# Optimization experiments

Measured on AMD Instinct MI355X. Metric: run time of the kernel, lower is better.

## Reference

```python
import jax, jax.numpy as jnp
import numpy as np

N_HEAD = 16
EPS = 1e-5


def setup_inputs() -> dict:
    key = jax.random.key(0)
    ks = jax.random.split(key, 9)
    B, T, C = 2, 1024, 1024
    s = 0.02
    return {
        "x": jax.random.normal(ks[0], (B, T, C), jnp.float32),
        "Wq": jax.random.normal(ks[1], (C, C), jnp.float32) * s,
        "Wk": jax.random.normal(ks[2], (C, C), jnp.float32) * s,
        "Wv": jax.random.normal(ks[3], (C, C), jnp.float32) * s,
        "Wq2": jax.random.normal(ks[4], (C, C), jnp.float32) * s,
        "Wk2": jax.random.normal(ks[5], (C, C), jnp.float32) * s,
        "Wo": jax.random.normal(ks[6], (C, C), jnp.float32) * s,
        "mixture": jnp.full((1,), -5.0, jnp.float32),  # quartet_gate_init
        "quartet_scale": jnp.ones((1,), jnp.float32),
    }


def reference(x, Wq, Wk, Wv, Wq2, Wk2, Wo, mixture, quartet_scale):
    B, T, C = x.shape
    H = N_HEAD
    Dh = C // H
    scale = 1.0 / jnp.sqrt(jnp.asarray(Dh, x.dtype))

    def heads(W):
        # torch Linear: y = x @ W.T ; then view(B,T,H,Dh).transpose(1,2)
        return (x @ W.T).reshape(B, T, H, Dh).transpose(0, 2, 1, 3)  # [B,H,T,Dh]

    q, k, v = heads(Wq), heads(Wk), heads(Wv)
    q2, k2 = heads(Wq2), heads(Wk2)

    qk = jnp.einsum("bhqd,bhkd->bhqk", q, k) * scale      # [B,H,T,T]
    q2k2 = jnp.einsum("bhqd,bhkd->bhqk", q2, k2) * scale  # [B,H,T,T]

    def row_norm(s):
        mu = s.mean(axis=-1, keepdims=True)
        sigma = s.std(axis=-1, keepdims=True, ddof=1)  # torch std is unbiased
        return (s - mu) / (sigma + EPS)

    qk_n = row_norm(qk)
    q2k2_n = row_norm(q2k2)
    m = jax.nn.sigmoid(mixture)  # [1], broadcasts
    scores = (1.0 - m) * qk_n + m * (qk_n * q2k2_n) * quartet_scale

    causal = jnp.tril(jnp.ones((T, T), bool))  # [T,T]
    scores = jnp.where(causal, scores, -jnp.inf)
    attn = jax.nn.softmax(scores, axis=-1)  # [B,H,T,T]

    y = jnp.einsum("bhqk,bhkd->bhqd", attn, v)  # [B,H,T,Dh]
    y = y.transpose(0, 2, 1, 3).reshape(B, T, C)
    return y @ Wo.T
```

## Files before the change

kernel.cpp:

```cpp
#include <hip/hip_runtime.h>
#include <hip/hip_bf16.h>
#include <stdint.h>

#define TS 1024
#define CS 1024
#define NH 16
#define DHEAD 64
#define NBATCH 2
#define EPSV 1e-5f
#define MEG 1048576

typedef __bf16 bf16x8 __attribute__((ext_vector_type(8)));
typedef float  f32x4  __attribute__((ext_vector_type(4)));

#define MFMA(a, b, c) __builtin_amdgcn_mfma_f32_16x16x32_bf16((a), (b), (c), 0, 0, 0)

__device__ __forceinline__ float bf2f(ushort u){
  union { uint32_t i; float f; } v; v.i = ((uint32_t)u) << 16; return v.f;
}
__device__ __forceinline__ ushort f2bf(float f){
  union { float f; uint32_t i; } v; v.f = f;
  uint32_t r = v.i + 0x7FFFu + ((v.i >> 16) & 1u);
  return (ushort)(r >> 16);
}

__device__ __forceinline__ void gl_lds16(const ushort* g, ushort* l) {
  __builtin_amdgcn_global_load_lds(
      (const __attribute__((address_space(1))) void*)g,
      (__attribute__((address_space(3))) void*)l, 16, 0, 0);
}

__global__ __launch_bounds__(256)
void cast_all(const float* __restrict__ x,
              const float* __restrict__ Wq, const float* __restrict__ Wk,
              const float* __restrict__ Wv, const float* __restrict__ Wq2,
              const float* __restrict__ Wk2, const float* __restrict__ Wo,
              ushort* __restrict__ xb, ushort* __restrict__ wcat)
{
  const int XC = 524288, TOT = 2097152;
  for (int idx = blockIdx.x * 256 + threadIdx.x; idx < TOT; idx += 524288) {
    const float* s; ushort* d; int c;
    if (idx < XC) { s = x; d = xb; c = idx; }
    else {
      int r = idx - XC; int w = r >> 18; c = r & 262143;
      switch (w) {
        case 0:  s = Wq;  d = wcat;           break;
        case 1:  s = Wk;  d = wcat + 1*MEG;   break;
        case 2:  s = Wv;  d = wcat + 4*MEG;   break;
        case 3:  s = Wq2; d = wcat + 2*MEG;   break;
        case 4:  s = Wk2; d = wcat + 3*MEG;   break;
        default: s = Wo;  d = wcat + 5*MEG;   break;
      }
    }
    float4 v = *(const float4*)(s + (size_t)c * 4);
    ushort4 o; o.x = f2bf(v.x); o.y = f2bf(v.y); o.z = f2bf(v.z); o.w = f2bf(v.w);
    *(ushort4*)(d + (size_t)c * 4) = o;
  }
}

#define BM 128
#define BN 128
#define BKK 32

__global__ __launch_bounds__(256, 2)
void gemm_proj(const ushort* __restrict__ A, const ushort* __restrict__ Bt,
               ushort* __restrict__ qb, ushort* __restrict__ kb,
               ushort* __restrict__ q2b, ushort* __restrict__ k2b,
               ushort* __restrict__ vtb,
               ushort* __restrict__ ktb, ushort* __restrict__ k2tb)
{
  __shared__ ushort a_s[BM * BKK];
  __shared__ ushort b_s[BN * BKK];

  const int n0 = blockIdx.x * BN;
  const int m0 = blockIdx.y * BM;

  const int t  = threadIdx.x;
  const int w  = t >> 6, l = t & 63;
  const int wr = w >> 1, wc = w & 1;
  const int l15 = l & 15, l4 = l >> 4;

  const int rs = l >> 2;
  const int c8 = (l & 3) * 8;

  f32x4 acc[4][4] = {};

  for (int k0 = 0; k0 < CS; k0 += BKK) {
    #pragma unroll
    for (int j = 0; j < 2; ++j) {
      int ch = w * 2 + j;
      int r  = ch * 16 + rs;
      gl_lds16(&A [(size_t)(m0 + r) * CS + k0 + c8], &a_s[ch * 512]);
      gl_lds16(&Bt[(size_t)(n0 + r) * CS + k0 + c8], &b_s[ch * 512]);
    }
    __syncthreads();

    bf16x8 af[4], bfr[4];
    #pragma unroll
    for (int mi = 0; mi < 4; ++mi)
      af[mi] = *(const bf16x8*)&a_s[(wr * 64 + mi * 16 + l15) * BKK + l4 * 8];
    #pragma unroll
    for (int ni = 0; ni < 4; ++ni)
      bfr[ni] = *(const bf16x8*)&b_s[(wc * 64 + ni * 16 + l15) * BKK + l4 * 8];

    #pragma unroll
    for (int mi = 0; mi < 4; ++mi)
      #pragma unroll
      for (int ni = 0; ni < 4; ++ni)
        acc[mi][ni] = MFMA(af[mi], bfr[ni], acc[mi][ni]);

    __syncthreads();
  }

  #pragma unroll
  for (int mi = 0; mi < 4; ++mi) {
    #pragma unroll
    for (int ni = 0; ni < 4; ++ni) {
      int col  = n0 + wc * 64 + ni * 16 + l15;
      int row0 = m0 + wr * 64 + mi * 16 + l4 * 4;
      int seg  = col >> 10, cc = col & (CS - 1);
      if (seg < 4) {
        ushort* dst = (seg == 0) ? qb : (seg == 1) ? kb : (seg == 2) ? q2b : k2b;
        float sc = (seg & 1) ? 1.f : 0.125f;
        #pragma unroll
        for (int e = 0; e < 4; ++e)
          dst[(size_t)(row0 + e) * CS + cc] = f2bf(acc[mi][ni][e] * sc);
        if (seg == 1 || seg == 3) {
          int bb = row0 >> 10, tt = row0 & (TS - 1);
          int hh = cc >> 6, dd = cc & (DHEAD - 1);
          ushort* td = (seg == 1) ? ktb : k2tb;
          ushort4 o;
          o.x = f2bf(acc[mi][ni][0]); o.y = f2bf(acc[mi][ni][1]);
          o.z = f2bf(acc[mi][ni][2]); o.w = f2bf(acc[mi][ni][3]);
          *(ushort4*)&td[(((size_t)(bb * NH + hh) * DHEAD + dd) * TS) + tt] = o;
        }
      } else {
        int bb = row0 >> 10, tt = row0 & (TS - 1);
        int hh = cc >> 6, dd = cc & (DHEAD - 1);
        ushort4 o;
        o.x = f2bf(acc[mi][ni][0]); o.y = f2bf(acc[mi][ni][1]);
        o.z = f2bf(acc[mi][ni][2]); o.w = f2bf(acc[mi][ni][3]);
        *(ushort4*)&vtb[(((size_t)(bb * NH + hh) * DHEAD + dd) * TS) + tt] = o;
      }
    }
  }
}

__global__ __launch_bounds__(256, 2)
void gemm_out(const ushort* __restrict__ A, const ushort* __restrict__ Bt,
              float* __restrict__ C)
{
  __shared__ ushort a_s[64 * BKK];
  __shared__ ushort b_s[128 * BKK];

  const int n0 = blockIdx.x * 128;
  const int m0 = blockIdx.y * 64;

  const int t  = threadIdx.x;
  const int w  = t >> 6, l = t & 63;
  const int l15 = l & 15, l4 = l >> 4;
  const int rs = l >> 2;
  const int c8 = (l & 3) * 8;

  f32x4 acc[8] = {};

  for (int k0 = 0; k0 < CS; k0 += BKK) {
    gl_lds16(&A[(size_t)(m0 + w * 16 + rs) * CS + k0 + c8], &a_s[w * 512]);
    #pragma unroll
    for (int j = 0; j < 2; ++j) {
      int ch = w * 2 + j;
      gl_lds16(&Bt[(size_t)(n0 + ch * 16 + rs) * CS + k0 + c8], &b_s[ch * 512]);
    }
    __syncthreads();

    bf16x8 af = *(const bf16x8*)&a_s[(w * 16 + l15) * BKK + l4 * 8];
    #pragma unroll
    for (int ni = 0; ni < 8; ++ni) {
      bf16x8 bfr = *(const bf16x8*)&b_s[(ni * 16 + l15) * BKK + l4 * 8];
      acc[ni] = MFMA(af, bfr, acc[ni]);
    }
    __syncthreads();
  }

  #pragma unroll
  for (int ni = 0; ni < 8; ++ni)
    #pragma unroll
    for (int e = 0; e < 4; ++e)
      C[(size_t)(m0 + w * 16 + l4 * 4 + e) * CS + n0 + ni * 16 + l15] = acc[ni][e];
}

__global__ __launch_bounds__(256, 2)
void gram(const ushort* __restrict__ ktb, const ushort* __restrict__ k2tb,
          ushort* __restrict__ g1b, ushort* __restrict__ g2b,
          float* __restrict__ csb)
{
  __shared__ ushort t_s[64 * 128];

  const int mat = blockIdx.x & 1, z = blockIdx.x >> 1;
  const ushort* S = (mat ? k2tb : ktb) + (size_t)z * DHEAD * TS;

  const int t = threadIdx.x, w = t >> 6, l = t & 63;
  const int l15 = l & 15, l4 = l >> 4;

  f32x4 acc[4] = {};
  float csacc = 0.f;

  for (int tt = 0; tt < 8; ++tt) {
    const int t0 = tt * 128;
    __syncthreads();
    #pragma unroll
    for (int i = 0; i < 4; ++i) {
      int issue = w * 4 + i;
      int row = issue * 4 + l4;
      int gs  = l15 ^ (row & 15);
      gl_lds16(&S[(size_t)row * TS + t0 + gs * 8], &t_s[issue * 512]);
    }
    __syncthreads();

    {
      int r = w * 16 + l15;
      #pragma unroll
      for (int j = 0; j < 4; ++j) {
        int gg = ((l4 * 4 + j) ^ (r & 15)) * 8;
        uint4 vv = *(const uint4*)&t_s[r * 128 + gg];
        const ushort* pu = (const ushort*)&vv;
        #pragma unroll
        for (int e2 = 0; e2 < 8; ++e2) csacc += bf2f(pu[e2]);
      }
    }

    #pragma unroll
    for (int ks = 0; ks < 4; ++ks) {
      int ar = w * 16 + l15;
      bf16x8 af = *(const bf16x8*)&t_s[ar * 128 + ((ks * 4 + l4) ^ (ar & 15)) * 8];
      #pragma unroll
      for (int ni = 0; ni < 4; ++ni) {
        int br = ni * 16 + l15;
        bf16x8 bf_ = *(const bf16x8*)&t_s[br * 128 + ((ks * 4 + l4) ^ (br & 15)) * 8];
        acc[ni] = MFMA(af, bf_, acc[ni]);
      }
    }
  }

  csacc += __shfl_xor(csacc, 16);
  csacc += __shfl_xor(csacc, 32);
  if (l4 == 0)
    csb[(mat * 32 + z) * 64 + w * 16 + l15] = csacc;

  ushort* G = (mat ? g2b : g1b) + (size_t)z * 4096;
  #pragma unroll
  for (int ni = 0; ni < 4; ++ni)
    #pragma unroll
    for (int e = 0; e < 4; ++e)
      G[(w * 16 + l4 * 4 + e) * 64 + ni * 16 + l15] = f2bf(acc[ni][e]);
}

__global__ __launch_bounds__(256, 3)
void attn_fused(const ushort* __restrict__ qb, const ushort* __restrict__ kb,
                const ushort* __restrict__ q2b, const ushort* __restrict__ k2b,
                const ushort* __restrict__ vtb, ushort* __restrict__ yb,
                const ushort* __restrict__ g1b, const ushort* __restrict__ g2b,
                const float* __restrict__ csb,
                const float* __restrict__ mixture, const float* __restrict__ qsc)
{
  __shared__ ushort kbuf [2][4096];
  __shared__ ushort k2buf[2][4096];
  __shared__ ushort vbuf [4096];
  __shared__ ushort p_s  [2 * 32 * 40];

  const int idx  = blockIdx.x;
  const int pp   = idx >> 8;
  const int base = idx & 255;
  const int xcd  = base & 7;
  const int mm   = base >> 3;
  const int qq   = mm & 7;
  const int z    = (mm >> 3) * 8 + xcd;
  const int q32  = 31 - (pp * 8 + qq);
  const int b    = z >> 4, h = z & 15;
  const int m0   = q32 * 32;
  const int nkv  = (q32 >> 1) + 1;

  const ushort* Q  = qb  + (size_t)b * TS * CS + h * DHEAD;
  const ushort* Q2 = q2b + (size_t)b * TS * CS + h * DHEAD;
  const ushort* K  = kb  + (size_t)b * TS * CS + h * DHEAD;
  const ushort* K2 = k2b + (size_t)b * TS * CS + h * DHEAD;
  const ushort* Vt = vtb + (size_t)z * DHEAD * TS;
  const ushort* G1 = g1b + (size_t)z * 4096;
  const ushort* G2 = g2b + (size_t)z * 4096;
  ushort* Y = yb + (size_t)b * TS * CS + h * DHEAD;

  const int t = threadIdx.x, w = t >> 6, l = t & 63;
  const int l15 = l & 15, l4 = l >> 4;
  const int r8 = l >> 3, g7 = l & 7;
  const int p  = w >> 1, wr = w & 1;
  const int qrow = wr * 16 + l15;

  const float L2E = 1.44269504f;
  const float gm = 1.f / (1.f + __expf(-mixture[0]));
  const float mq2 = gm * qsc[0] * L2E;
  const float om2 = (1.f - gm) * L2E;

  auto stage_k = [&](int ti, int bs) {
    const int t0 = ti * 64;
    #pragma unroll
    for (int i = 0; i < 2; ++i) {
      int issue = w * 2 + i;
      int row = issue * 8 + r8;
      int gs  = g7 ^ (row & 7);
      gl_lds16(&K [(size_t)(t0 + row) * CS + gs * 8], &kbuf [bs][issue * 512]);
      gl_lds16(&K2[(size_t)(t0 + row) * CS + gs * 8], &k2buf[bs][issue * 512]);
    }
  };
  auto stage_v = [&](int ti) {
    const int t0 = ti * 64;
    #pragma unroll
    for (int i = 0; i < 2; ++i) {
      int issue = w * 2 + i;
      int row = issue * 8 + r8;
      int gs  = g7 ^ (row & 7);
      gl_lds16(&Vt[(size_t)row * TS + t0 + gs * 8], &vbuf[issue * 512]);
    }
  };

  {
    int row = w * 8 + r8;
    int gs  = g7 ^ (row & 7);
    gl_lds16(&Q [(size_t)(m0 + row) * CS + gs * 8], &vbuf[w * 512]);
    gl_lds16(&Q2[(size_t)(m0 + row) * CS + gs * 8], &vbuf[2048 + w * 512]);
  }
  stage_k(0, 0);
  __syncthreads();

  bf16x8 fq[2], fq2[2];
  #pragma unroll
  for (int ks = 0; ks < 2; ++ks) {
    int gg = ((ks * 4 + l4) ^ (qrow & 7)) * 8;
    fq [ks] = *(const bf16x8*)&vbuf[qrow * 64 + gg];
    fq2[ks] = *(const bf16x8*)&vbuf[2048 + qrow * 64 + gg];
  }

  f32x4 U1[4] = {}, U2[4] = {};
  #pragma unroll
  for (int ks = 0; ks < 2; ++ks)
    #pragma unroll
    for (int ni = 0; ni < 4; ++ni) {
      bf16x8 bg = *(const bf16x8*)&G1[(ni * 16 + l15) * 64 + ks * 32 + l4 * 8];
      U1[ni] = MFMA(bg, fq[ks], U1[ni]);
    }
  #pragma unroll
  for (int ks = 0; ks < 2; ++ks)
    #pragma unroll
    for (int ni = 0; ni < 4; ++ni) {
      bf16x8 bg = *(const bf16x8*)&G2[(ni * 16 + l15) * 64 + ks * 32 + l4 * 8];
      U2[ni] = MFMA(bg, fq2[ks], U2[ni]);
    }

  float ssq1 = 0.f, md1 = 0.f, ssq2 = 0.f, md2 = 0.f;
  #pragma unroll
  for (int ni = 0; ni < 4; ++ni) {
    int gsq = (ni * 2 + (l4 >> 1)) ^ (qrow & 7);
    int off = qrow * 64 + gsq * 8 + (l4 & 1) * 4;
    ushort qa[4], qb2[4];
    *(uint2*)qa  = *(const uint2*)&vbuf[off];
    *(uint2*)qb2 = *(const uint2*)&vbuf[2048 + off];
    float c1[4], c2[4];
    *(float4*)c1 = *(const float4*)&csb[z * 64 + ni * 16 + l4 * 4];
    *(float4*)c2 = *(const float4*)&csb[2048 + z * 64 + ni * 16 + l4 * 4];
    #pragma unroll
    for (int e = 0; e < 4; ++e) {
      float qv1 = bf2f(qa[e]), qv2 = bf2f(qb2[e]);
      ssq1 = fmaf(U1[ni][e], qv1, ssq1); md1 = fmaf(qv1, c1[e], md1);
      ssq2 = fmaf(U2[ni][e], qv2, ssq2); md2 = fmaf(qv2, c2[e], md2);
    }
  }
  ssq1 += __shfl_xor(ssq1, 16); md1 += __shfl_xor(md1, 16);
  ssq2 += __shfl_xor(ssq2, 16); md2 += __shfl_xor(md2, 16);
  ssq1 += __shfl_xor(ssq1, 32); md1 += __shfl_xor(md1, 32);
  ssq2 += __shfl_xor(ssq2, 32); md2 += __shfl_xor(md2, 32);

  const float mu1 = md1 * (1.f / TS), mu2 = md2 * (1.f / TS);
  const float va1 = (ssq1 - (float)TS * mu1 * mu1) * (1.f / (TS - 1));
  const float va2 = (ssq2 - (float)TS * mu2 * mu2) * (1.f / (TS - 1));
  const float iv1 = 1.f / (sqrtf(fmaxf(va1, 0.f)) + EPSV);
  const float iv2 = 1.f / (sqrtf(fmaxf(va2, 0.f)) + EPSV);
  __syncthreads();

  float lrow = 0.f;
  f32x4 accO[4] = {};

  for (int i = 0; i < nkv; ++i) {
    const int t0 = i * 64;
    stage_v(i);
    if (i + 1 < nkv) stage_k(i + 1, (i + 1) & 1);

    const ushort* ks_ = kbuf [i & 1];
    const ushort* k2s_= k2buf[i & 1];

    f32x4 a1[2] = {}, a2[2] = {};
    #pragma unroll
    for (int ks = 0; ks < 2; ++ks) {
      bf16x8 bk[2], bk2[2];
      #pragma unroll
      for (int ni = 0; ni < 2; ++ni) {
        int j  = p * 32 + ni * 16 + l15;
        int gg = ((ks * 4 + l4) ^ (j & 7)) * 8;
        bk [ni] = *(const bf16x8*)&ks_ [j * 64 + gg];
        bk2[ni] = *(const bf16x8*)&k2s_[j * 64 + gg];
      }
      #pragma unroll
      for (int ni = 0; ni < 2; ++ni) {
        a1[ni] = MFMA(bk [ni], fq [ks], a1[ni]);
        a2[ni] = MFMA(bk2[ni], fq2[ks], a2[ni]);
      }
    }

    const int grow = m0 + qrow;
    #pragma unroll
    for (int ni = 0; ni < 2; ++ni) {
      float pe[4];
      #pragma unroll
      for (int e = 0; e < 4; ++e) {
        float n1 = (a1[ni][e] - mu1) * iv1;
        float n2 = (a2[ni][e] - mu2) * iv2;
        float sc = n1 * fmaf(mq2, n2, om2);
        float pv = exp2f(sc);
        int gcol = t0 + p * 32 + ni * 16 + l4 * 4 + e;
        pv = (gcol <= grow) ? pv : 0.f;
        lrow += pv;
        pe[e] = pv;
      }
      uint32_t pk01, pk23;
      asm("v_cvt_pk_bf16_f32 %0, %1, %2" : "=v"(pk01) : "v"(pe[0]), "v"(pe[1]));
      asm("v_cvt_pk_bf16_f32 %0, %1, %2" : "=v"(pk23) : "v"(pe[2]), "v"(pe[3]));
      uint2 pk; pk.x = pk01; pk.y = pk23;
      *(uint2*)&p_s[p * 1280 + qrow * 40 + ni * 16 + l4 * 4] = pk;
    }

    __syncthreads();

    {
      bf16x8 ap = *(const bf16x8*)&p_s[p * 1280 + qrow * 40 + l4 * 8];
      #pragma unroll
      for (int ni = 0; ni < 4; ++ni) {
        int d  = ni * 16 + l15;
        int gg = (((p * 4 + l4)) ^ (d & 7)) * 8;
        bf16x8 bv = *(const bf16x8*)&vbuf[d * 64 + gg];
        accO[ni] = MFMA(ap, bv, accO[ni]);
      }
    }

    __syncthreads();
  }

  lrow += __shfl_xor(lrow, 16);
  lrow += __shfl_xor(lrow, 32);

  float* fb = (float*)kbuf;
  float* fl = (float*)k2buf;
  if (p == 1) {
    #pragma unroll
    for (int ni = 0; ni < 4; ++ni)
      #pragma unroll
      for (int e = 0; e < 4; ++e)
        fb[(wr * 16 + l4 * 4 + e) * 64 + ni * 16 + l15] = accO[ni][e];
    if (l4 == 0) fl[qrow] = lrow;
  }
  __syncthreads();
  if (p == 0) {
    float lt = lrow + fl[qrow];
    float il[4];
    #pragma unroll
    for (int e = 0; e < 4; ++e)
      il[e] = 1.f / __shfl(lt, l4 * 4 + e);
    #pragma unroll
    for (int ni = 0; ni < 4; ++ni)
      #pragma unroll
      for (int e = 0; e < 4; ++e) {
        float o = accO[ni][e] + fb[(wr * 16 + l4 * 4 + e) * 64 + ni * 16 + l15];
        Y[(size_t)(m0 + wr * 16 + l4 * 4 + e) * CS + ni * 16 + l15] = f2bf(o * il[e]);
      }
  }
}

extern "C" void kernel_launch(void* const* d_in, const int* in_sizes, int n_in,
                              void* d_out, int out_size, void* d_ws, size_t ws_size,
                              hipStream_t stream) {
  const float* x    = (const float*)d_in[0];
  const float* Wq   = (const float*)d_in[1];
  const float* Wk   = (const float*)d_in[2];
  const float* Wv   = (const float*)d_in[3];
  const float* Wq2  = (const float*)d_in[4];
  const float* Wk2  = (const float*)d_in[5];
  const float* Wo   = (const float*)d_in[6];
  const float* mixture = (const float*)d_in[7];
  const float* qsc  = (const float*)d_in[8];
  float* out = (float*)d_out;

  const size_t MT = (size_t)NBATCH * TS;
  ushort* ws = (ushort*)d_ws;
  ushort* xb   = ws;
  ushort* wcat = xb   + (size_t)2 * MEG;
  ushort* qb   = wcat + (size_t)6 * MEG;
  ushort* q2b  = qb   + (size_t)2 * MEG;
  ushort* kb   = q2b  + (size_t)2 * MEG;
  ushort* k2b  = kb   + (size_t)2 * MEG;
  ushort* vtb  = k2b  + (size_t)2 * MEG;
  ushort* yb   = vtb  + (size_t)2 * MEG;
  ushort* ktb  = yb   + (size_t)2 * MEG;
  ushort* k2tb = ktb  + (size_t)2 * MEG;
  ushort* g1b  = k2tb + (size_t)2 * MEG;
  ushort* g2b  = g1b  + (size_t)(MEG / 8);
  float*  csb  = (float*)(g2b + (size_t)(MEG / 8));
  ushort* wob  = wcat + (size_t)5 * MEG;

  cast_all<<<2048, 256, 0, stream>>>(x, Wq, Wk, Wv, Wq2, Wk2, Wo, xb, wcat);

  gemm_proj<<<dim3(5 * CS / BN, MT / BM, 1), 256, 0, stream>>>(
      xb, wcat, qb, kb, q2b, k2b, vtb, ktb, k2tb);

  gram<<<64, 256, 0, stream>>>(ktb, k2tb, g1b, g2b, csb);

  attn_fused<<<1024, 256, 0, stream>>>(qb, kb, q2b, k2b, vtb, yb,
                                       g1b, g2b, csb, mixture, qsc);

  gemm_out<<<dim3(8, 32), 256, 0, stream>>>(yb, wob, out);
}
```

Baseline: 108.8 us.

## Widen GEMM K-tile with swizzled LDS and double-buffer V in attention

The projection GEMM now stages a 64-wide K slice per iteration using XOR-swizzled LDS layout, which halves the number of barrier pairs and is meant to reduce bank conflicts. In the attention kernel, V is double-buffered and prefetched alongside the next K/K2 tile, and the staging of Q/Q2 is moved into p_s and kbuf[1]. The barrier between writing P and the PV MFMA is dropped, relying on each wave reading only its own P rows. LDS use grows by 8 KB per attention block, which could pressure the 3-blocks-per-CU occupancy target.

```diff
diff --git a/kernel.cpp b/kernel.cpp
--- a/kernel.cpp
+++ b/kernel.cpp
@@ -69,8 +69,8 @@
                ushort* __restrict__ vtb,
                ushort* __restrict__ ktb, ushort* __restrict__ k2tb)
 {
-  __shared__ ushort a_s[BM * BKK];
-  __shared__ ushort b_s[BN * BKK];
+  __shared__ ushort a_s[BM * 64];
+  __shared__ ushort b_s[BN * 64];
 
   const int n0 = blockIdx.x * BN;
   const int m0 = blockIdx.y * BM;
@@ -79,35 +79,42 @@
   const int w  = t >> 6, l = t & 63;
   const int wr = w >> 1, wc = w & 1;
   const int l15 = l & 15, l4 = l >> 4;
-
-  const int rs = l >> 2;
-  const int c8 = (l & 3) * 8;
+  const int r8 = l >> 3, g7 = l & 7;
 
   f32x4 acc[4][4] = {};
 
-  for (int k0 = 0; k0 < CS; k0 += BKK) {
-    #pragma unroll
-    for (int j = 0; j < 2; ++j) {
-      int ch = w * 2 + j;
-      int r  = ch * 16 + rs;
-      gl_lds16(&A [(size_t)(m0 + r) * CS + k0 + c8], &a_s[ch * 512]);
-      gl_lds16(&Bt[(size_t)(n0 + r) * CS + k0 + c8], &b_s[ch * 512]);
-    }
-    __syncthreads();
-
-    bf16x8 af[4], bfr[4];
-    #pragma unroll
-    for (int mi = 0; mi < 4; ++mi)
-      af[mi] = *(const bf16x8*)&a_s[(wr * 64 + mi * 16 + l15) * BKK + l4 * 8];
-    #pragma unroll
-    for (int ni = 0; ni < 4; ++ni)
-      bfr[ni] = *(const bf16x8*)&b_s[(wc * 64 + ni * 16 + l15) * BKK + l4 * 8];
-
-    #pragma unroll
-    for (int mi = 0; mi < 4; ++mi)
-      #pragma unroll
-      for (int ni = 0; ni < 4; ++ni)
-        acc[mi][ni] = MFMA(af[mi], bfr[ni], acc[mi][ni]);
+  for (int k0 = 0; k0 < CS; k0 += 64) {
+    #pragma unroll
+    for (int i = 0; i < 4; ++i) {
+      int issue = w * 4 + i;
+      int row   = issue * 8 + r8;
+      int gs    = g7 ^ (row & 7);
+      gl_lds16(&A [(size_t)(m0 + row) * CS + k0 + gs * 8], &a_s[issue * 512]);
+      gl_lds16(&Bt[(size_t)(n0 + row) * CS + k0 + gs * 8], &b_s[issue * 512]);
+    }
+    __syncthreads();
+
+    #pragma unroll
+    for (int ks = 0; ks < 2; ++ks) {
+      bf16x8 af[4], bfr[4];
+      #pragma unroll
+      for (int mi = 0; mi < 4; ++mi) {
+        int row = wr * 64 + mi * 16 + l15;
+        int gl  = (ks * 4 + l4) ^ (row & 7);
+        af[mi] = *(const bf16x8*)&a_s[row * 64 + gl * 8];
+      }
+      #pragma unroll
+      for (int ni = 0; ni < 4; ++ni) {
+        int row = wc * 64 + ni * 16 + l15;
+        int gl  = (ks * 4 + l4) ^ (row & 7);
+        bfr[ni] = *(const bf16x8*)&b_s[row * 64 + gl * 8];
+      }
+      #pragma unroll
+      for (int mi = 0; mi < 4; ++mi)
+        #pragma unroll
+        for (int ni = 0; ni < 4; ++ni)
+          acc[mi][ni] = MFMA(af[mi], bfr[ni], acc[mi][ni]);
+    }
 
     __syncthreads();
   }
@@ -265,7 +272,7 @@
 {
   __shared__ ushort kbuf [2][4096];
   __shared__ ushort k2buf[2][4096];
-  __shared__ ushort vbuf [4096];
+  __shared__ ushort vbuf [2][4096];
   __shared__ ushort p_s  [2 * 32 * 40];
 
   const int idx  = blockIdx.x;
@@ -311,32 +318,33 @@
       gl_lds16(&K2[(size_t)(t0 + row) * CS + gs * 8], &k2buf[bs][issue * 512]);
     }
   };
-  auto stage_v = [&](int ti) {
+  auto stage_v = [&](int ti, int bs) {
     const int t0 = ti * 64;
     #pragma unroll
     for (int i = 0; i < 2; ++i) {
       int issue = w * 2 + i;
       int row = issue * 8 + r8;
       int gs  = g7 ^ (row & 7);
-      gl_lds16(&Vt[(size_t)row * TS + t0 + gs * 8], &vbuf[issue * 512]);
+      gl_lds16(&Vt[(size_t)row * TS + t0 + gs * 8], &vbuf[bs][issue * 512]);
     }
   };
 
   {
     int row = w * 8 + r8;
     int gs  = g7 ^ (row & 7);
-    gl_lds16(&Q [(size_t)(m0 + row) * CS + gs * 8], &vbuf[w * 512]);
-    gl_lds16(&Q2[(size_t)(m0 + row) * CS + gs * 8], &vbuf[2048 + w * 512]);
+    gl_lds16(&Q [(size_t)(m0 + row) * CS + gs * 8], &p_s[w * 512]);
+    gl_lds16(&Q2[(size_t)(m0 + row) * CS + gs * 8], &kbuf[1][w * 512]);
   }
   stage_k(0, 0);
+  stage_v(0, 0);
   __syncthreads();
 
   bf16x8 fq[2], fq2[2];
   #pragma unroll
   for (int ks = 0; ks < 2; ++ks) {
     int gg = ((ks * 4 + l4) ^ (qrow & 7)) * 8;
-    fq [ks] = *(const bf16x8*)&vbuf[qrow * 64 + gg];
-    fq2[ks] = *(const bf16x8*)&vbuf[2048 + qrow * 64 + gg];
+    fq [ks] = *(const bf16x8*)&p_s[qrow * 64 + gg];
+    fq2[ks] = *(const bf16x8*)&kbuf[1][qrow * 64 + gg];
   }
 
   f32x4 U1[4] = {}, U2[4] = {};
@@ -361,8 +369,8 @@
     int gsq = (ni * 2 + (l4 >> 1)) ^ (qrow & 7);
     int off = qrow * 64 + gsq * 8 + (l4 & 1) * 4;
     ushort qa[4], qb2[4];
-    *(uint2*)qa  = *(const uint2*)&vbuf[off];
-    *(uint2*)qb2 = *(const uint2*)&vbuf[2048 + off];
+    *(uint2*)qa  = *(const uint2*)&p_s[off];
+    *(uint2*)qb2 = *(const uint2*)&kbuf[1][off];
     float c1[4], c2[4];
     *(float4*)c1 = *(const float4*)&csb[z * 64 + ni * 16 + l4 * 4];
     *(float4*)c2 = *(const float4*)&csb[2048 + z * 64 + ni * 16 + l4 * 4];
@@ -389,12 +397,12 @@
   f32x4 accO[4] = {};
 
   for (int i = 0; i < nkv; ++i) {
-    const int t0 = i * 64;
-    stage_v(i);
-    if (i + 1 < nkv) stage_k(i + 1, (i + 1) & 1);
-
-    const ushort* ks_ = kbuf [i & 1];
-    const ushort* k2s_= k2buf[i & 1];
+    const int t0  = i * 64;
+    const int cur = i & 1;
+    if (i + 1 < nkv) { stage_k(i + 1, cur ^ 1); stage_v(i + 1, cur ^ 1); }
+
+    const ushort* ks_ = kbuf [cur];
+    const ushort* k2s_= k2buf[cur];
 
     f32x4 a1[2] = {}, a2[2] = {};
     #pragma unroll
@@ -436,15 +444,13 @@
       *(uint2*)&p_s[p * 1280 + qrow * 40 + ni * 16 + l4 * 4] = pk;
     }
 
-    __syncthreads();
-
     {
       bf16x8 ap = *(const bf16x8*)&p_s[p * 1280 + qrow * 40 + l4 * 8];
       #pragma unroll
       for (int ni = 0; ni < 4; ++ni) {
         int d  = ni * 16 + l15;
-        int gg = (((p * 4 + l4)) ^ (d & 7)) * 8;
-        bf16x8 bv = *(const bf16x8*)&vbuf[d * 64 + gg];
+        int gg = ((p * 4 + l4) ^ (d & 7)) * 8;
+        bf16x8 bv = *(const bf16x8*)&vbuf[cur][d * 64 + gg];
         accO[ni] = MFMA(ap, bv, accO[ni]);
       }
     }
```

After: 105.9 us. -2.7%, faster.
